# Kernel tuning notes

Hardware: AMD Instinct MI355X
Metric: run time of the kernel (lower is better)

## Reference

```python
import jax, jax.numpy as jnp
import numpy as np

NUM_HEADS = 16
ROPE_BASE = 10000.0
NEG_INF = float('-inf')


def _rotate_half_interleaved(x):
    # x: [..., d]; interleaved rotation: (-x2, x1) pairs
    x1 = x[..., ::2]
    x2 = x[..., 1::2]
    return jnp.stack((-x2, x1), axis=-1).reshape(x.shape)


def _rope_tables(seq_len, head_dim, dtype):
    inv_freq = 1.0 / (ROPE_BASE ** (jnp.arange(0, head_dim, 2, dtype=jnp.float32) / head_dim))
    pos = jnp.arange(seq_len, dtype=jnp.float32)
    freqs = pos[:, None] * inv_freq[None, :]          # [S, d/2]
    emb = jnp.concatenate((freqs, freqs), axis=-1)    # [S, d]  (HF-style concat, as in source)
    return jnp.cos(emb).astype(dtype), jnp.sin(emb).astype(dtype)


def setup_inputs() -> dict:
    key = jax.random.key(0)
    ks = jax.random.split(key, 4)
    B, S, H = 2, 2048, 2048
    scale = 0.02
    x = jax.random.normal(ks[0], (B, S, H), dtype=jnp.float32)
    qkv_w = jax.random.normal(ks[1], (3 * H, H), dtype=jnp.float32) * scale
    qkv_b = jnp.zeros((3 * H,), dtype=jnp.float32)
    out_w = jax.random.normal(ks[2], (H, H), dtype=jnp.float32) * scale
    out_b = jnp.zeros((H,), dtype=jnp.float32)
    attention_mask = jnp.ones((B, S), dtype=jnp.int32)
    return {"x": x, "attention_mask": attention_mask, "qkv_w": qkv_w,
            "qkv_b": qkv_b, "out_w": out_w, "out_b": out_b}


def reference(x, attention_mask, qkv_w, qkv_b, out_w, out_b):
    B, S, H = x.shape
    nh = NUM_HEADS
    hd = H // nh
    scale = hd ** -0.5

    qkv = x @ qkv_w.T + qkv_b                            # [B,S,3H]
    qkv = qkv.reshape(B, S, 3, nh, hd).transpose(2, 0, 3, 1, 4)  # [3,B,nh,S,hd]
    q, k, v = qkv[0], qkv[1], qkv[2]

    cos, sin = _rope_tables(S, hd, x.dtype)              # [S,hd]
    cos = cos[None, None, :, :]
    sin = sin[None, None, :, :]
    q = q * cos + _rotate_half_interleaved(q) * sin
    k = k * cos + _rotate_half_interleaved(k) * sin

    scores = jnp.einsum('bhqd,bhkd->bhqk', q, k) * scale  # [B,nh,S,S]
    causal = jnp.triu(jnp.ones((S, S), dtype=bool), k=1)
    scores = jnp.where(causal[None, None], NEG_INF, scores)
    key_mask = (attention_mask == 0)[:, None, None, :]    # [B,1,1,S]
    scores = jnp.where(key_mask, NEG_INF, scores)

    weights = jax.nn.softmax(scores, axis=-1)
    attn = jnp.einsum('bhqk,bhkd->bhqd', weights, v)       # [B,nh,S,hd]
    attn = attn.transpose(0, 2, 1, 3).reshape(B, S, H)
    return attn @ out_w.T + out_b
```

## Files before the change

kernel.cpp:

```cpp
#include <hip/hip_runtime.h>

typedef __bf16 bf16;
typedef __bf16 bf16x2 __attribute__((ext_vector_type(2)));
typedef __bf16 bf16x4 __attribute__((ext_vector_type(4)));
typedef __bf16 bf16x8 __attribute__((ext_vector_type(8)));
typedef float f32x4 __attribute__((ext_vector_type(4)));
typedef float f32x16 __attribute__((ext_vector_type(16)));

#define MFMA_BF16(a, b, c) __builtin_amdgcn_mfma_f32_16x16x32_bf16(a, b, c, 0, 0, 0)
#define MFMA32(a, b, c)    __builtin_amdgcn_mfma_f32_32x32x16_bf16(a, b, c, 0, 0, 0)

__device__ __forceinline__ void async16(const void* g, void* l) {
    __builtin_amdgcn_global_load_lds(
        (const __attribute__((address_space(1))) void*)g,
        (__attribute__((address_space(3))) void*)l,
        16, 0, 0);
}

__device__ __forceinline__ unsigned pack2(float a, float b) {
    bf16x2 t; t[0] = (bf16)a; t[1] = (bf16)b;
    return __builtin_bit_cast(unsigned, t);
}

__device__ __forceinline__ void cvt8_body(const float* __restrict__ in,
                                          bf16* __restrict__ out, int blk) {
    int i = (blk * 256 + (int)threadIdx.x) * 8;
    float4 a = *(const float4*)(in + i);
    float4 b = *(const float4*)(in + i + 4);
    bf16x8 o;
    o[0] = (bf16)a.x; o[1] = (bf16)a.y; o[2] = (bf16)a.z; o[3] = (bf16)a.w;
    o[4] = (bf16)b.x; o[5] = (bf16)b.y; o[6] = (bf16)b.z; o[7] = (bf16)b.w;
    *(bf16x8*)(out + i) = o;
}

__global__ void prep(const float* __restrict__ x, const float* __restrict__ qkvw,
                     const float* __restrict__ outw, const int* __restrict__ am,
                     bf16* __restrict__ xb, bf16* __restrict__ wqkv, bf16* __restrict__ wout,
                     float* __restrict__ cosT, float* __restrict__ sinT,
                     float* __restrict__ mbias) {
    int blk = blockIdx.x;
    if (blk < 4096)        cvt8_body(x,    xb,   blk);
    else if (blk < 10240)  cvt8_body(qkvw, wqkv, blk - 4096);
    else if (blk < 12288)  cvt8_body(outw, wout, blk - 10240);
    else {
        int i = (blk - 12288) * 256 + threadIdx.x;
        int s = i >> 7, d = i & 127, fi = d & 63;
        float inv = exp2f(-(float)fi * (13.287712379549449f / 64.0f));
        float ang = (float)s * inv;
        cosT[i] = cosf(ang);
        sinT[i] = sinf(ang);
        if (i < 2 * 2048) mbias[i] = (am[i] == 0) ? -1.4427e30f : 0.0f;
    }
}

template <int EPI>
__global__ void __launch_bounds__(256, 2)
gemm_bt(const bf16* __restrict__ A, const bf16* __restrict__ Bt,
        const float* __restrict__ bias, float* __restrict__ Cf,
        bf16* __restrict__ qb, bf16* __restrict__ kb, bf16* __restrict__ vtb,
        const float* __restrict__ cosT, const float* __restrict__ sinT,
        int M, int N, int K) {
    __shared__ __align__(16) bf16 sA[128 * 64];
    __shared__ __align__(16) bf16 sB[128 * 64];
    const int tid  = threadIdx.x;
    const int lane = tid & 63;
    const int quad = lane >> 4, l15 = lane & 15;
    const int wid = tid >> 6, wm = wid >> 1, wn = wid & 1;
    const int bm = blockIdx.x, bn = blockIdx.y;

    f32x4 acc[4][4];
#pragma unroll
    for (int i = 0; i < 4; i++)
#pragma unroll
        for (int j = 0; j < 4; j++)
#pragma unroll
            for (int c = 0; c < 4; c++) acc[i][j][c] = 0.0f;

    const int r0 = tid >> 3, x0 = tid & 7;
    const int g0 = x0 ^ (r0 & 7);
    const bf16* pa = A  + (size_t)(bm * 128 + r0) * K + g0 * 8;
    const bf16* pb = Bt + (size_t)(bn * 128 + r0) * K + g0 * 8;
    bf16* la = sA + tid * 8;
    bf16* lb = sB + tid * 8;
    const size_t gstep = (size_t)32 * K;

    for (int k0 = 0; k0 < K; k0 += 64) {
#pragma unroll
        for (int i = 0; i < 4; i++) {
            async16(pa + i * gstep, la + i * 2048);
            async16(pb + i * gstep, lb + i * 2048);
        }
        pa += 64; pb += 64;
        __syncthreads();
#pragma unroll
        for (int ks = 0; ks < 2; ks++) {
            bf16x8 af[4], bfr[4];
#pragma unroll
            for (int i = 0; i < 4; i++) {
                int r = wm * 64 + i * 16 + l15;
                int x = (ks * 4 + quad) ^ (r & 7);
                af[i] = *(const bf16x8*)(sA + r * 64 + x * 8);
            }
#pragma unroll
            for (int i = 0; i < 4; i++) {
                int r = wn * 64 + i * 16 + l15;
                int x = (ks * 4 + quad) ^ (r & 7);
                bfr[i] = *(const bf16x8*)(sB + r * 64 + x * 8);
            }
#pragma unroll
            for (int mi = 0; mi < 4; mi++)
#pragma unroll
                for (int ni = 0; ni < 4; ni++)
                    acc[mi][ni] = MFMA_BF16(af[mi], bfr[ni], acc[mi][ni]);
        }
        __syncthreads();
    }

    if (EPI == 0) {
#pragma unroll
        for (int mi = 0; mi < 4; mi++)
#pragma unroll
            for (int ni = 0; ni < 4; ni++) {
                int row0 = bm * 128 + wm * 64 + mi * 16 + quad * 4;
                int col  = bn * 128 + wn * 64 + ni * 16 + l15;
                float bv = bias[col];
#pragma unroll
                for (int r = 0; r < 4; r++)
                    Cf[(size_t)(row0 + r) * N + col] = acc[mi][ni][r] + bv;
            }
    } else {
#pragma unroll
        for (int mi = 0; mi < 4; mi++)
#pragma unroll
            for (int ni = 0; ni < 4; ni++) {
                int col   = bn * 128 + wn * 64 + ni * 16 + l15;
                int which = col >> 11;
                int hcol  = col & 2047;
                int h = hcol >> 7, d = hcol & 127;
                float bv = bias[col];
#pragma unroll
                for (int r = 0; r < 4; r++) {
                    int row = bm * 128 + wm * 64 + mi * 16 + quad * 4 + r;
                    int b = row >> 11, s = row & 2047;
                    float v  = acc[mi][ni][r] + bv;
                    float vp = __shfl_xor(v, 1, 64);
                    float ov = v;
                    if (which < 2) {
                        float c  = cosT[(s << 7) + d];
                        float sn = sinT[(s << 7) + d];
                        ov = v * c + ((d & 1) ? vp : -vp) * sn;
                    }
                    if (which == 0) ov *= 0.12751743f;
                    size_t bh = (size_t)(b * 16 + h);
                    if (which == 0)      qb[(bh * 2048 + s) * 128 + d] = (bf16)ov;
                    else if (which == 1) kb[(bh * 2048 + s) * 128 + d] = (bf16)ov;
                    else                 vtb[(bh * 128 + d) * 2048 + s] = (bf16)ov;
                }
            }
    }
}

__global__ void __launch_bounds__(256, 2)
fattn(const bf16* __restrict__ Q, const bf16* __restrict__ Kg,
      const bf16* __restrict__ Vt, const float* __restrict__ mbias,
      bf16* __restrict__ O, float* __restrict__ Opart, float* __restrict__ mlpart) {
    __shared__ __align__(16) bf16 sK[2][64 * 128];
    __shared__ __align__(16) bf16 sV[2][128 * 64];
    const int tid = threadIdx.x, lane = tid & 63, w = tid >> 6;
    const int l31 = lane & 31, half = lane >> 5;
    const int id = (int)blockIdx.x;
    const int bh = id & 31, v = id >> 5;
    const int p = v >> 1, role = v & 1;
    const int qa = 15 - p;
    const int n1 = role ? (15 - 2 * p) : 17;

    const bf16* Qb  = Q  + (size_t)bh * 2048 * 128;
    const bf16* Kbh = Kg + (size_t)bh * 2048 * 128;
    const bf16* Vbh = Vt + (size_t)bh * 128 * 2048;
    const int b = bh >> 4, hh = bh & 15;
    const float* mbb = mbias + b * 2048;

    const int swk = (l31 & 15) ^ (l31 >> 4);
    const int swv = (l31 & 7) ^ ((l31 >> 3) & 3);
    const int rk = tid >> 4, xk = tid & 15, gkb = xk ^ rk;
    const int rv = tid >> 3, xv = tid & 7;
    const int gv = xv ^ (rv & 7) ^ ((rv >> 3) & 3);

    auto KT = [&](int t) { return role ? (t < n1 ? 17 + t : t - n1) : t; };

    int qt = qa;
    int myq  = qt * 128 + w * 32 + l31;
    int qmin = qt * 128 + w * 32;

    bf16x8 qf[8];
#pragma unroll
    for (int kq = 0; kq < 8; kq++)
        qf[kq] = *(const bf16x8*)(Qb + (size_t)myq * 128 + kq * 16 + half * 8);

    f32x16 oacc[4];
#pragma unroll
    for (int dt = 0; dt < 4; dt++)
#pragma unroll
        for (int c = 0; c < 16; c++) oacc[dt][c] = 0.0f;
    float m_s = -3e38f, l_s = 0.0f;

    {
        int kb0 = KT(0) * 64;
#pragma unroll
        for (int i = 0; i < 4; i++) {
            async16(Kbh + (size_t)(kb0 + rk + i * 16) * 128 + (gkb ^ (i & 1)) * 8,
                    &sK[0][(i * 256 + tid) * 8]);
            async16(Vbh + (size_t)(rv + i * 32) * 2048 + kb0 + gv * 8,
                    &sV[0][(i * 256 + tid) * 8]);
        }
    }
    __syncthreads();

    for (int t = 0; t < 17; t++) {
        if (role && t == n1) {
            float lf = l_s + __shfl_xor(l_s, 32, 64);
            size_t slot = (size_t)(bh * 8 + (qa - 8)) * 2 + 1;
            float* op = Opart + slot * 16384 + (size_t)(w * 32 + l31) * 128;
#pragma unroll
            for (int dt = 0; dt < 4; dt++)
#pragma unroll
                for (int g = 0; g < 4; g++) {
                    float4 o4 = make_float4(oacc[dt][g * 4 + 0], oacc[dt][g * 4 + 1],
                                            oacc[dt][g * 4 + 2], oacc[dt][g * 4 + 3]);
                    *(float4*)(op + dt * 32 + 8 * g + 4 * half) = o4;
                }
            if (half == 0) {
                float* mp = mlpart + (slot * 128 + (w * 32 + l31)) * 2;
                mp[0] = m_s; mp[1] = lf;
            }
#pragma unroll
            for (int dt = 0; dt < 4; dt++)
#pragma unroll
                for (int c = 0; c < 16; c++) oacc[dt][c] = 0.0f;
            m_s = -3e38f; l_s = 0.0f;
            qt = p;
            myq  = qt * 128 + w * 32 + l31;
            qmin = qt * 128 + w * 32;
#pragma unroll
            for (int kq = 0; kq < 8; kq++)
                qf[kq] = *(const bf16x8*)(Qb + (size_t)myq * 128 + kq * 16 + half * 8);
        }

        const int kb0 = KT(t) * 64;
        const int buf = t & 1;
        if (t + 1 < 17) {
            const int nb0 = KT(t + 1) * 64;
#pragma unroll
            for (int i = 0; i < 4; i++) {
                async16(Kbh + (size_t)(nb0 + rk + i * 16) * 128 + (gkb ^ (i & 1)) * 8,
                        &sK[buf ^ 1][(i * 256 + tid) * 8]);
                async16(Vbh + (size_t)(rv + i * 32) * 2048 + nb0 + gv * 8,
                        &sV[buf ^ 1][(i * 256 + tid) * 8]);
            }
        }
        const bf16* sKb = sK[buf];
        const bf16* sVb = sV[buf];

        f32x16 sacc[2];
#pragma unroll
        for (int tt = 0; tt < 2; tt++)
#pragma unroll
            for (int c = 0; c < 16; c++) sacc[tt][c] = 0.0f;
#pragma unroll
        for (int kq = 0; kq < 8; kq++) {
#pragma unroll
            for (int tt = 0; tt < 2; tt++) {
                int row = tt * 32 + l31;
                int x = (kq * 2 + half) ^ swk;
                bf16x8 kf = *(const bf16x8*)(sKb + row * 128 + x * 8);
                sacc[tt] = MFMA32(kf, qf[kq], sacc[tt]);
            }
        }

        float mx = -3e38f;
        if (kb0 + 63 < qmin) {
#pragma unroll
            for (int tt = 0; tt < 2; tt++)
#pragma unroll
                for (int g = 0; g < 4; g++) {
                    float4 mb4 = *(const float4*)(mbb + kb0 + tt * 32 + 8 * g + 4 * half);
#pragma unroll
                    for (int r2 = 0; r2 < 4; r2++) {
                        float vv = sacc[tt][g * 4 + r2] + ((const float*)&mb4)[r2];
                        sacc[tt][g * 4 + r2] = vv;
                        mx = fmaxf(mx, vv);
                    }
                }
        } else {
#pragma unroll
            for (int tt = 0; tt < 2; tt++)
#pragma unroll
                for (int g = 0; g < 4; g++) {
                    float4 mb4 = *(const float4*)(mbb + kb0 + tt * 32 + 8 * g + 4 * half);
#pragma unroll
                    for (int r2 = 0; r2 < 4; r2++) {
                        int sk = kb0 + tt * 32 + 8 * g + 4 * half + r2;
                        float vv = sacc[tt][g * 4 + r2] + ((const float*)&mb4)[r2];
                        vv = (sk > myq) ? -1e30f : vv;
                        sacc[tt][g * 4 + r2] = vv;
                        mx = fmaxf(mx, vv);
                    }
                }
        }

        mx = fmaxf(mx, __shfl_xor(mx, 32, 64));
        float mnew  = fmaxf(m_s, mx);
        float alpha = exp2f(m_s - mnew);
        float rs = 0.0f;
#pragma unroll
        for (int tt = 0; tt < 2; tt++)
#pragma unroll
            for (int c = 0; c < 16; c++) {
                float pe = exp2f(sacc[tt][c] - mnew);
                sacc[tt][c] = pe;
                rs += pe;
            }
        l_s = l_s * alpha + rs;
        m_s = mnew;
#pragma unroll
        for (int dt = 0; dt < 4; dt++) oacc[dt] *= alpha;

#pragma unroll
        for (int tt = 0; tt < 2; tt++) {
            unsigned w8[8];
#pragma unroll
            for (int i = 0; i < 8; i++)
                w8[i] = pack2(sacc[tt][2 * i], sacc[tt][2 * i + 1]);
#pragma unroll
            for (int s2 = 0; s2 < 2; s2++) {
                const int bse = 4 * s2;
                unsigned a0 = half ? w8[bse]     : w8[bse + 2];
                unsigned a1 = half ? w8[bse + 1] : w8[bse + 3];
                unsigned z0 = (unsigned)__shfl_xor((int)a0, 32, 64);
                unsigned z1 = (unsigned)__shfl_xor((int)a1, 32, 64);
                union { unsigned u[4]; bf16x8 vv; } pu;
                pu.u[0] = half ? z0 : w8[bse];
                pu.u[1] = half ? z1 : w8[bse + 1];
                pu.u[2] = half ? w8[bse + 2] : z0;
                pu.u[3] = half ? w8[bse + 3] : z1;
                bf16x8 pf = pu.vv;
                const int c = (tt * 2 + s2) * 2 + half;
#pragma unroll
                for (int dt = 0; dt < 4; dt++) {
                    int row = dt * 32 + l31;
                    int x = c ^ swv;
                    bf16x8 vf = *(const bf16x8*)(sVb + row * 64 + x * 8);
                    oacc[dt] = MFMA32(vf, pf, oacc[dt]);
                }
            }
        }
        __syncthreads();
    }

    float lf = l_s + __shfl_xor(l_s, 32, 64);
    if (role == 0) {
        size_t slot = (size_t)(bh * 8 + (qa - 8)) * 2 + 0;
        float* op = Opart + slot * 16384 + (size_t)(w * 32 + l31) * 128;
#pragma unroll
        for (int dt = 0; dt < 4; dt++)
#pragma unroll
            for (int g = 0; g < 4; g++) {
                float4 o4 = make_float4(oacc[dt][g * 4 + 0], oacc[dt][g * 4 + 1],
                                        oacc[dt][g * 4 + 2], oacc[dt][g * 4 + 3]);
                *(float4*)(op + dt * 32 + 8 * g + 4 * half) = o4;
            }
        if (half == 0) {
            float* mp = mlpart + (slot * 128 + (w * 32 + l31)) * 2;
            mp[0] = m_s; mp[1] = lf;
        }
    } else {
        float inv = 1.0f / lf;
        size_t base = ((size_t)(b * 2048 + myq)) * 2048 + hh * 128;
#pragma unroll
        for (int dt = 0; dt < 4; dt++)
#pragma unroll
            for (int g = 0; g < 4; g++) {
                bf16x4 o4;
#pragma unroll
                for (int r2 = 0; r2 < 4; r2++) o4[r2] = (bf16)(oacc[dt][g * 4 + r2] * inv);
                *(bf16x4*)(O + base + dt * 32 + 8 * g + 4 * half) = o4;
            }
    }
}

__global__ void combine(const float* __restrict__ Opart, const float* __restrict__ mlpart,
                        bf16* __restrict__ attn) {
    int i = blockIdx.x * 256 + threadIdx.x;
    int dq = (i & 31) * 4;
    int row = i >> 5;
    int qloc = row & 127, ba = row >> 7;
    int ai = ba & 7, bh = ba >> 3;
    const float* mlA = mlpart + ((size_t)(ba * 2 + 0) * 128 + qloc) * 2;
    const float* mlB = mlpart + ((size_t)(ba * 2 + 1) * 128 + qloc) * 2;
    float mA = mlA[0], lA = mlA[1], mB = mlB[0], lB = mlB[1];
    float m = fmaxf(mA, mB);
    float wA = exp2f(mA - m), wB = exp2f(mB - m);
    float inv = 1.0f / (wA * lA + wB * lB);
    float4 oA = *(const float4*)(Opart + (size_t)(ba * 2 + 0) * 16384 + qloc * 128 + dq);
    float4 oB = *(const float4*)(Opart + (size_t)(ba * 2 + 1) * 16384 + qloc * 128 + dq);
    int q = (8 + ai) * 128 + qloc;
    int b = bh >> 4, hh = bh & 15;
    bf16x4 o4;
    o4[0] = (bf16)((wA * oA.x + wB * oB.x) * inv);
    o4[1] = (bf16)((wA * oA.y + wB * oB.y) * inv);
    o4[2] = (bf16)((wA * oA.z + wB * oB.z) * inv);
    o4[3] = (bf16)((wA * oA.w + wB * oB.w) * inv);
    *(bf16x4*)(attn + ((size_t)(b * 2048 + q)) * 2048 + hh * 128 + dq) = o4;
}

extern "C" void kernel_launch(void* const* d_in, const int* in_sizes, int n_in,
                              void* d_out, int out_size, void* d_ws, size_t ws_size,
                              hipStream_t stream) {
    const float* x     = (const float*)d_in[0];
    const int*   am    = (const int*)d_in[1];
    const float* qkvw  = (const float*)d_in[2];
    const float* qkvb  = (const float*)d_in[3];
    const float* outw  = (const float*)d_in[4];
    const float* outb  = (const float*)d_in[5];
    float* out = (float*)d_out;

    char* ws = (char*)d_ws;
    bf16*  xb    = (bf16*)(ws);
    bf16*  wqkv  = (bf16*)(ws + (16ull << 20));
    bf16*  wout  = (bf16*)(ws + (40ull << 20));
    bf16*  qb    = (bf16*)(ws + (48ull << 20));
    bf16*  kb    = (bf16*)(ws + (64ull << 20));
    bf16*  vtb   = (bf16*)(ws + (80ull << 20));
    bf16*  attn  = (bf16*)(ws + (96ull << 20));
    float* cosT  = (float*)(ws + (112ull << 20));
    float* sinT  = (float*)(ws + (113ull << 20));
    float* mbias = (float*)(ws + (114ull << 20));
    float* Opart  = (float*)(ws);
    float* mlpart = (float*)(ws + (32ull << 20));

    prep<<<13312, 256, 0, stream>>>(x, qkvw, outw, am, xb, wqkv, wout, cosT, sinT, mbias);

    gemm_bt<1><<<dim3(32, 48), 256, 0, stream>>>(
        xb, wqkv, qkvb, nullptr, qb, kb, vtb, cosT, sinT, 4096, 6144, 2048);

    fattn<<<dim3(512), 256, 0, stream>>>(qb, kb, vtb, mbias, attn, Opart, mlpart);

    combine<<<4096, 256, 0, stream>>>(Opart, mlpart, attn);

    gemm_bt<0><<<dim3(32, 16), 256, 0, stream>>>(
        attn, wout, outb, out, nullptr, nullptr, nullptr, nullptr, nullptr,
        4096, 2048, 2048);
}
```

Baseline: 371.8 us.

## Replace GEMM with 256x256-tile 512-thread kernel using triple-buffered async loads

Both projection GEMMs now use a 256x256 output tile computed by 8 waves, with a K-step of 32 and a three-stage LDS ring filled by async global-to-LDS loads. Explicit vmcnt waits and a single barrier per iteration let the next tiles load while MFMAs run, and s_setprio raises priority around the MFMA bursts. The larger tile gives more reuse per byte loaded and removes one of the two barriers per K-step. In exchange the grid is much smaller, especially for the output projection (128 blocks), and register and LDS pressure rise.

```diff
diff --git a/kernel.cpp b/kernel.cpp
--- a/kernel.cpp
+++ b/kernel.cpp
@@ -54,75 +54,104 @@
 }
 
 template <int EPI>
-__global__ void __launch_bounds__(256, 2)
-gemm_bt(const bf16* __restrict__ A, const bf16* __restrict__ Bt,
+__global__ void __launch_bounds__(512, 2)
+gemm256(const bf16* __restrict__ A, const bf16* __restrict__ Bt,
         const float* __restrict__ bias, float* __restrict__ Cf,
         bf16* __restrict__ qb, bf16* __restrict__ kb, bf16* __restrict__ vtb,
         const float* __restrict__ cosT, const float* __restrict__ sinT,
-        int M, int N, int K) {
-    __shared__ __align__(16) bf16 sA[128 * 64];
-    __shared__ __align__(16) bf16 sB[128 * 64];
+        int N, int K) {
+    __shared__ __align__(16) bf16 sA[3][8192];
+    __shared__ __align__(16) bf16 sB[3][8192];
     const int tid  = threadIdx.x;
     const int lane = tid & 63;
     const int quad = lane >> 4, l15 = lane & 15;
-    const int wid = tid >> 6, wm = wid >> 1, wn = wid & 1;
+    const int wid = tid >> 6, wm = wid >> 2, wn = wid & 3;
     const int bm = blockIdx.x, bn = blockIdx.y;
 
-    f32x4 acc[4][4];
-#pragma unroll
-    for (int i = 0; i < 4; i++)
+    f32x4 acc[8][4];
+#pragma unroll
+    for (int i = 0; i < 8; i++)
 #pragma unroll
         for (int j = 0; j < 4; j++)
 #pragma unroll
             for (int c = 0; c < 4; c++) acc[i][j][c] = 0.0f;
 
-    const int r0 = tid >> 3, x0 = tid & 7;
-    const int g0 = x0 ^ (r0 & 7);
-    const bf16* pa = A  + (size_t)(bm * 128 + r0) * K + g0 * 8;
-    const bf16* pb = Bt + (size_t)(bn * 128 + r0) * K + g0 * 8;
-    bf16* la = sA + tid * 8;
-    bf16* lb = sB + tid * 8;
-    const size_t gstep = (size_t)32 * K;
-
-    for (int k0 = 0; k0 < K; k0 += 64) {
-#pragma unroll
-        for (int i = 0; i < 4; i++) {
-            async16(pa + i * gstep, la + i * 2048);
-            async16(pb + i * gstep, lb + i * 2048);
-        }
-        pa += 64; pb += 64;
-        __syncthreads();
-#pragma unroll
-        for (int ks = 0; ks < 2; ks++) {
-            bf16x8 af[4], bfr[4];
-#pragma unroll
-            for (int i = 0; i < 4; i++) {
-                int r = wm * 64 + i * 16 + l15;
-                int x = (ks * 4 + quad) ^ (r & 7);
-                af[i] = *(const bf16x8*)(sA + r * 64 + x * 8);
-            }
-#pragma unroll
-            for (int i = 0; i < 4; i++) {
-                int r = wn * 64 + i * 16 + l15;
-                int x = (ks * 4 + quad) ^ (r & 7);
-                bfr[i] = *(const bf16x8*)(sB + r * 64 + x * 8);
-            }
-#pragma unroll
-            for (int mi = 0; mi < 4; mi++)
-#pragma unroll
-                for (int ni = 0; ni < 4; ni++)
-                    acc[mi][ni] = MFMA_BF16(af[mi], bfr[ni], acc[mi][ni]);
-        }
-        __syncthreads();
+    const int srow  = tid >> 2;
+    const int sswz8 = ((tid & 3) ^ (srow & 3)) * 8;
+    const bf16* pa0 = A  + (size_t)(bm * 256 + srow) * K + sswz8;
+    const bf16* pa1 = pa0 + (size_t)128 * K;
+    const bf16* pb0 = Bt + (size_t)(bn * 256 + srow) * K + sswz8;
+    const bf16* pb1 = pb0 + (size_t)128 * K;
+
+    bf16 *aX = sA[0], *aY = sA[1], *aZ = sA[2];
+    bf16 *bX = sB[0], *bY = sB[1], *bZ = sB[2];
+
+    const int xoff = (quad ^ (l15 & 3)) * 8;
+    const int arow = wm * 128 + l15;
+    const int brow = wn * 64 + l15;
+
+    auto stage = [&](bf16* la, bf16* lb) {
+        async16(pa0, la + tid * 8);
+        async16(pa1, la + 4096 + tid * 8);
+        async16(pb0, lb + tid * 8);
+        async16(pb1, lb + 4096 + tid * 8);
+        pa0 += 32; pa1 += 32; pb0 += 32; pb1 += 32;
+    };
+
+    auto compute = [&](const bf16* la, const bf16* lb) {
+        bf16x8 bfv[4], afv[4];
+#pragma unroll
+        for (int i = 0; i < 4; i++)
+            bfv[i] = *(const bf16x8*)(lb + (brow + i * 16) * 32 + xoff);
+#pragma unroll
+        for (int i = 0; i < 4; i++)
+            afv[i] = *(const bf16x8*)(la + (arow + i * 16) * 32 + xoff);
+        __builtin_amdgcn_s_setprio(1);
+#pragma unroll
+        for (int mi = 0; mi < 4; mi++)
+#pragma unroll
+            for (int ni = 0; ni < 4; ni++)
+                acc[mi][ni] = MFMA_BF16(afv[mi], bfv[ni], acc[mi][ni]);
+        __builtin_amdgcn_s_setprio(0);
+#pragma unroll
+        for (int i = 0; i < 4; i++)
+            afv[i] = *(const bf16x8*)(la + (arow + 64 + i * 16) * 32 + xoff);
+        __builtin_amdgcn_s_setprio(1);
+#pragma unroll
+        for (int mi = 0; mi < 4; mi++)
+#pragma unroll
+            for (int ni = 0; ni < 4; ni++)
+                acc[mi + 4][ni] = MFMA_BF16(afv[mi], bfv[ni], acc[mi + 4][ni]);
+        __builtin_amdgcn_s_setprio(0);
+    };
+
+    stage(aX, bX);
+    stage(aY, bY);
+    asm volatile("s_waitcnt vmcnt(4)" ::: "memory");
+    __builtin_amdgcn_s_barrier();
+    __builtin_amdgcn_sched_barrier(0);
+
+    const int NT = K >> 5;
+    for (int t = 0; t < NT; ++t) {
+        if (t + 2 < NT) stage(aZ, bZ);
+        compute(aX, bX);
+        if (t + 1 < NT) {
+            if (t + 2 < NT) asm volatile("s_waitcnt vmcnt(4)" ::: "memory");
+            else            asm volatile("s_waitcnt vmcnt(0)" ::: "memory");
+            __builtin_amdgcn_s_barrier();
+            __builtin_amdgcn_sched_barrier(0);
+        }
+        bf16* t0 = aX; aX = aY; aY = aZ; aZ = t0;
+        bf16* t1 = bX; bX = bY; bY = bZ; bZ = t1;
     }
 
     if (EPI == 0) {
 #pragma unroll
-        for (int mi = 0; mi < 4; mi++)
+        for (int mi = 0; mi < 8; mi++)
 #pragma unroll
             for (int ni = 0; ni < 4; ni++) {
-                int row0 = bm * 128 + wm * 64 + mi * 16 + quad * 4;
-                int col  = bn * 128 + wn * 64 + ni * 16 + l15;
+                int row0 = bm * 256 + wm * 128 + mi * 16 + quad * 4;
+                int col  = bn * 256 + wn * 64 + ni * 16 + l15;
                 float bv = bias[col];
 #pragma unroll
                 for (int r = 0; r < 4; r++)
@@ -130,17 +159,17 @@
             }
     } else {
 #pragma unroll
-        for (int mi = 0; mi < 4; mi++)
+        for (int mi = 0; mi < 8; mi++)
 #pragma unroll
             for (int ni = 0; ni < 4; ni++) {
-                int col   = bn * 128 + wn * 64 + ni * 16 + l15;
+                int col   = bn * 256 + wn * 64 + ni * 16 + l15;
                 int which = col >> 11;
                 int hcol  = col & 2047;
                 int h = hcol >> 7, d = hcol & 127;
                 float bv = bias[col];
 #pragma unroll
                 for (int r = 0; r < 4; r++) {
-                    int row = bm * 128 + wm * 64 + mi * 16 + quad * 4 + r;
+                    int row = bm * 256 + wm * 128 + mi * 16 + quad * 4 + r;
                     int b = row >> 11, s = row & 2047;
                     float v  = acc[mi][ni][r] + bv;
                     float vp = __shfl_xor(v, 1, 64);
@@ -440,14 +469,14 @@
 
     prep<<<13312, 256, 0, stream>>>(x, qkvw, outw, am, xb, wqkv, wout, cosT, sinT, mbias);
 
-    gemm_bt<1><<<dim3(32, 48), 256, 0, stream>>>(
-        xb, wqkv, qkvb, nullptr, qb, kb, vtb, cosT, sinT, 4096, 6144, 2048);
+    gemm256<1><<<dim3(16, 24), 512, 0, stream>>>(
+        xb, wqkv, qkvb, nullptr, qb, kb, vtb, cosT, sinT, 6144, 2048);
 
     fattn<<<dim3(512), 256, 0, stream>>>(qb, kb, vtb, mbias, attn, Opart, mlpart);
 
     combine<<<4096, 256, 0, stream>>>(Opart, mlpart, attn);
 
-    gemm_bt<0><<<dim3(32, 16), 256, 0, stream>>>(
+    gemm256<0><<<dim3(16, 8), 512, 0, stream>>>(
         attn, wout, outb, out, nullptr, nullptr, nullptr, nullptr, nullptr,
-        4096, 2048, 2048);
-}
+        2048, 2048);
+}
```

New measurement: 502.5 us. +35.2%, slower.
